# Performance work log

Measured on AMD Instinct MI355X. Metric: run time of the kernel, lower is better.

## Reference

```python
import jax, jax.numpy as jnp
import numpy as np

K = 1_000_000      # number of sparse (2D-det, 3D-anchor) candidate pairs
ROWS = 200         # max 2D detections
COLS = 70400       # number of 3D anchors (200*176*2)
SENTINEL = -9999999.0


def setup_inputs() -> dict:
    key = jax.random.key(0)
    ks = jax.random.split(key, 12)
    input_1 = jax.random.normal(ks[0], (1, 4, 1, K), dtype=jnp.float32)
    idx0 = jax.random.randint(ks[1], (K,), 0, ROWS)
    idx1 = jax.random.randint(ks[2], (K,), 0, COLS)
    tensor_index = jnp.stack([idx0, idx1], axis=1).astype(jnp.int64)
    # fuse_2d_3d: 1x1 Conv2d stack 4->18->36->36->1 (weights as (out,in) matrices)
    def w(k, o, i):
        return jax.random.normal(k, (o, i), dtype=jnp.float32) * (1.0 / np.sqrt(i))
    return {
        "input_1": input_1,
        "tensor_index": tensor_index,
        "W1": w(ks[3], 18, 4),  "b1": jnp.zeros((18,), jnp.float32),
        "W2": w(ks[4], 36, 18), "b2": jnp.zeros((36,), jnp.float32),
        "W3": w(ks[5], 36, 36), "b3": jnp.zeros((36,), jnp.float32),
        "W4": w(ks[6], 1, 36),  "b4": jnp.zeros((1,), jnp.float32),
    }


def reference(input_1, tensor_index, W1, b1, W2, b2, W3, b3, W4, b4):
    # 1x1 convs over (1,4,1,K) are channel matmuls over the K pair axis.
    x = input_1[0, :, 0, :]                                   # (4, K)
    h = jax.nn.relu(jnp.dot(W1, x) + b1[:, None])             # (18, K)
    h = jax.nn.relu(jnp.dot(W2, h) + b2[:, None])             # (36, K)
    h = jax.nn.relu(jnp.dot(W3, h) + b3[:, None])             # (36, K)
    v = (jnp.dot(W4, h) + b4[:, None])[0]                     # (K,) fused score per pair
    # Scatter into dense sentinel-filled grid, then max-reduce the 200 dim
    # (equivalent to MaxPool2d([200,1]) in the original).
    dense = jnp.full((ROWS, COLS), SENTINEL, dtype=input_1.dtype)
    dense = dense.at[tensor_index[:, 0], tensor_index[:, 1]].max(v)
    out = jnp.max(dense, axis=0).reshape(1, -1, 1)            # (1, 70400, 1)
    flag = 1
    return (out, flag)
```

## Files before the change

kernel.cpp:

```cpp
#include <hip/hip_runtime.h>

#define KN 1000000
#define NCOLS 70400
#define NTILES (KN / 16)
#define NBLK 1024
#define NTHR 256

typedef _Float16 f16x8 __attribute__((ext_vector_type(8)));
typedef float    f32x4 __attribute__((ext_vector_type(4)));

__device__ __forceinline__ unsigned encodeF(float f) {
    unsigned b = __float_as_uint(f);
    return (b & 0x80000000u) ? ~b : (b | 0x80000000u);
}
__device__ __forceinline__ float decodeF(unsigned e) {
    unsigned b = (e & 0x80000000u) ? (e & 0x7fffffffu) : ~e;
    return __uint_as_float(b);
}
#define ENC_SENT 0x34E76980u

#define LGKM0() asm volatile("s_waitcnt lgkmcnt(0)" ::: "memory")


__global__ __launch_bounds__(NTHR)
__attribute__((amdgpu_waves_per_eu(4, 4)))
void mlp_scatter_mfma(const float* __restrict__ x, const int* __restrict__ tidx,
                      const float* __restrict__ W1, const float* __restrict__ b1,
                      const float* __restrict__ W2, const float* __restrict__ b2,
                      const float* __restrict__ W3, const float* __restrict__ b3,
                      const float* __restrict__ W4, const float* __restrict__ b4,
                      unsigned* __restrict__ outU)
{
    __shared__ _Float16 smem[4][1808];
    __shared__ float vt[4][16];

    const int lane = threadIdx.x & 63;
    const int wv   = threadIdx.x >> 6;
    const int quad = lane >> 4;
    const int n    = lane & 15;

    {
        unsigned* sp = (unsigned*)&smem[wv][0];
#pragma unroll
        for (int i = 0; i < 14; ++i) sp[i * 64 + lane] = 0u;
    }

    auto bf = [&](const float* W, int OUT, int IN, int t, int ks) {
        f16x8 r;
#pragma unroll
        for (int j = 0; j < 8; ++j) {
            int k  = ks * 32 + quad * 8 + j;
            int ng = t * 16 + n;
            float w = (ng < OUT && k < IN) ? W[ng * IN + k] : 0.0f;
            r[j] = (_Float16)w;
        }
        return r;
    };
    const f16x8 B1_0 = bf(W1, 18,  4, 0, 0), B1_1 = bf(W1, 18,  4, 1, 0);
    const f16x8 B2_0 = bf(W2, 36, 18, 0, 0), B2_1 = bf(W2, 36, 18, 1, 0), B2_2 = bf(W2, 36, 18, 2, 0);
    const f16x8 B3_00 = bf(W3, 36, 36, 0, 0), B3_01 = bf(W3, 36, 36, 0, 1);
    const f16x8 B3_10 = bf(W3, 36, 36, 1, 0), B3_11 = bf(W3, 36, 36, 1, 1);
    const f16x8 B3_20 = bf(W3, 36, 36, 2, 0), B3_21 = bf(W3, 36, 36, 2, 1);
    const f16x8 B4_0 = bf(W4,  1, 36, 0, 0), B4_1 = bf(W4,  1, 36, 0, 1);

    const float bias1_0 = b1[n];
    const float bias1_1 = (n < 2) ? b1[16 + n] : 0.0f;
    const float bias2_0 = b2[n], bias2_1 = b2[16 + n];
    const float bias2_2 = (n < 4) ? b2[32 + n] : 0.0f;
    const float bias3_0 = b3[n], bias3_1 = b3[16 + n];
    const float bias3_2 = (n < 4) ? b3[32 + n] : 0.0f;
    const float b4s = b4[0];

    _Float16* H1 = &smem[wv][0];
    _Float16* H2 = &smem[wv][640];

    const int gw = (blockIdx.x * blockDim.x + threadIdx.x) >> 6;
    const int nw = (gridDim.x * blockDim.x) >> 6;

    for (int tile = gw; tile < NTILES; tile += nw) {
        const int kb = tile * 16;

        const float xj0 = x[0 * KN + kb + n];
        const float xj1 = x[1 * KN + kb + n];
        const float xj2 = x[2 * KN + kb + n];
        const float xj3 = x[3 * KN + kb + n];
        f16x8 a1;
#pragma unroll
        for (int j = 0; j < 8; ++j) a1[j] = (_Float16)0.0f;
        if (quad == 0) {
            a1[0] = (_Float16)xj0; a1[1] = (_Float16)xj1;
            a1[2] = (_Float16)xj2; a1[3] = (_Float16)xj3;
        }

        const int col = ((const int2*)tidx)[kb + n].y;

        f32x4 c0 = {bias1_0, bias1_0, bias1_0, bias1_0};
        f32x4 c1 = {bias1_1, bias1_1, bias1_1, bias1_1};
        c0 = __builtin_amdgcn_mfma_f32_16x16x32_f16(a1, B1_0, c0, 0, 0, 0);
        c1 = __builtin_amdgcn_mfma_f32_16x16x32_f16(a1, B1_1, c1, 0, 0, 0);
#pragma unroll
        for (int r = 0; r < 4; ++r) {
            H1[(quad * 4 + r) * 40 + n]      = (_Float16)fmaxf(c0[r], 0.0f);
            H1[(quad * 4 + r) * 40 + 16 + n] = (_Float16)fmaxf(c1[r], 0.0f);
        }
        LGKM0();

        const f16x8 a2 = *(const f16x8*)&H1[n * 40 + quad * 8];
        f32x4 d0 = {bias2_0, bias2_0, bias2_0, bias2_0};
        f32x4 d1 = {bias2_1, bias2_1, bias2_1, bias2_1};
        f32x4 d2 = {bias2_2, bias2_2, bias2_2, bias2_2};
        d0 = __builtin_amdgcn_mfma_f32_16x16x32_f16(a2, B2_0, d0, 0, 0, 0);
        d1 = __builtin_amdgcn_mfma_f32_16x16x32_f16(a2, B2_1, d1, 0, 0, 0);
        d2 = __builtin_amdgcn_mfma_f32_16x16x32_f16(a2, B2_2, d2, 0, 0, 0);
#pragma unroll
        for (int r = 0; r < 4; ++r) {
            H2[(quad * 4 + r) * 72 + n]      = (_Float16)fmaxf(d0[r], 0.0f);
            H2[(quad * 4 + r) * 72 + 16 + n] = (_Float16)fmaxf(d1[r], 0.0f);
            H2[(quad * 4 + r) * 72 + 32 + n] = (_Float16)fmaxf(d2[r], 0.0f);
        }
        LGKM0();

        const f16x8 a30 = *(const f16x8*)&H2[n * 72 + quad * 8];
        const f16x8 a31 = *(const f16x8*)&H2[n * 72 + 32 + quad * 8];
        f32x4 e0 = {bias3_0, bias3_0, bias3_0, bias3_0};
        f32x4 e1 = {bias3_1, bias3_1, bias3_1, bias3_1};
        f32x4 e2 = {bias3_2, bias3_2, bias3_2, bias3_2};
        e0 = __builtin_amdgcn_mfma_f32_16x16x32_f16(a30, B3_00, e0, 0, 0, 0);
        e0 = __builtin_amdgcn_mfma_f32_16x16x32_f16(a31, B3_01, e0, 0, 0, 0);
        e1 = __builtin_amdgcn_mfma_f32_16x16x32_f16(a30, B3_10, e1, 0, 0, 0);
        e1 = __builtin_amdgcn_mfma_f32_16x16x32_f16(a31, B3_11, e1, 0, 0, 0);
        e2 = __builtin_amdgcn_mfma_f32_16x16x32_f16(a30, B3_20, e2, 0, 0, 0);
        e2 = __builtin_amdgcn_mfma_f32_16x16x32_f16(a31, B3_21, e2, 0, 0, 0);
        LGKM0();
#pragma unroll
        for (int r = 0; r < 4; ++r) {
            H2[(quad * 4 + r) * 72 + n]      = (_Float16)fmaxf(e0[r], 0.0f);
            H2[(quad * 4 + r) * 72 + 16 + n] = (_Float16)fmaxf(e1[r], 0.0f);
            H2[(quad * 4 + r) * 72 + 32 + n] = (_Float16)fmaxf(e2[r], 0.0f);
        }
        LGKM0();

        const f16x8 a40 = *(const f16x8*)&H2[n * 72 + quad * 8];
        const f16x8 a41 = *(const f16x8*)&H2[n * 72 + 32 + quad * 8];
        f32x4 f0 = {0.0f, 0.0f, 0.0f, 0.0f};
        f0 = __builtin_amdgcn_mfma_f32_16x16x32_f16(a40, B4_0, f0, 0, 0, 0);
        f0 = __builtin_amdgcn_mfma_f32_16x16x32_f16(a41, B4_1, f0, 0, 0, 0);

        if (n == 0) {
#pragma unroll
            for (int r = 0; r < 4; ++r) vt[wv][quad * 4 + r] = f0[r] + b4s;
        }
        LGKM0();
        const float v = vt[wv][n];
        const unsigned enc = encodeF(v) - ENC_SENT;
        if (lane < 16) atomicMax(&outU[col], enc);
    }
}

__global__ __launch_bounds__(256) void init_kernel(unsigned* __restrict__ outU) {
    int gid = blockIdx.x * blockDim.x + threadIdx.x;
    if (gid < NCOLS) outU[gid] = 0u;
}

__global__ __launch_bounds__(256) void decode_kernel(unsigned* __restrict__ outU,
                                                     int out_size) {
    int gid = blockIdx.x * blockDim.x + threadIdx.x;
    if (gid < out_size) {
        float r = (gid < NCOLS) ? decodeF(outU[gid] + ENC_SENT) : 1.0f;
        ((float*)outU)[gid] = r;
    }
}

extern "C" void kernel_launch(void* const* d_in, const int* in_sizes, int n_in,
                              void* d_out, int out_size, void* d_ws, size_t ws_size,
                              hipStream_t stream) {
    const float* x    = (const float*)d_in[0];
    const int*   tidx = (const int*)d_in[1];
    const float* W1 = (const float*)d_in[2];
    const float* b1 = (const float*)d_in[3];
    const float* W2 = (const float*)d_in[4];
    const float* b2 = (const float*)d_in[5];
    const float* W3 = (const float*)d_in[6];
    const float* b3 = (const float*)d_in[7];
    const float* W4 = (const float*)d_in[8];
    const float* b4 = (const float*)d_in[9];
    unsigned* outU = (unsigned*)d_out;

    init_kernel<<<(NCOLS + 255) / 256, 256, 0, stream>>>(outU);

    mlp_scatter_mfma<<<NBLK, NTHR, 0, stream>>>(
        x, tidx, W1, b1, W2, b2, W3, b3, W4, b4, outU);

    decode_kernel<<<(out_size + 255) / 256, 256, 0, stream>>>(outU, out_size);
}
```

Before: 141.0 us.

## Process two tiles per wave iteration with prefetch and shuffle-based final layer

Each wave now handles a pair of 16-row tiles per loop iteration, interleaving their MFMA chains to raise instruction-level parallelism. It also register-prefetches the next pair's inputs and column indices so global load latency overlaps the current compute. The 36->1 output layer moves off MFMA to per-lane FMAs plus a 16-lane xor-shuffle reduction, which drops the LDS round-trip for final scores and the explicit lgkmcnt waits. The cost is higher register pressure from the doubled accumulators and prefetch registers, under a fixed waves-per-EU setting.

```diff
diff --git a/kernel.cpp b/kernel.cpp
--- a/kernel.cpp
+++ b/kernel.cpp
@@ -2,7 +2,7 @@
 
 #define KN 1000000
 #define NCOLS 70400
-#define NTILES (KN / 16)
+#define NPAIRS (KN / 32)
 #define NBLK 1024
 #define NTHR 256
 
@@ -19,7 +19,7 @@
 }
 #define ENC_SENT 0x34E76980u
 
-#define LGKM0() asm volatile("s_waitcnt lgkmcnt(0)" ::: "memory")
+#define MFMA16(a, b, c) __builtin_amdgcn_mfma_f32_16x16x32_f16((a), (b), (c), 0, 0, 0)
 
 
 __global__ __launch_bounds__(NTHR)
@@ -31,18 +31,20 @@
                       const float* __restrict__ W4, const float* __restrict__ b4,
                       unsigned* __restrict__ outU)
 {
-    __shared__ _Float16 smem[4][1808];
-    __shared__ float vt[4][16];
+    __shared__ _Float16 smem[4][2][1152];
 
     const int lane = threadIdx.x & 63;
     const int wv   = threadIdx.x >> 6;
     const int quad = lane >> 4;
     const int n    = lane & 15;
 
-    {
-        unsigned* sp = (unsigned*)&smem[wv][0];
-#pragma unroll
-        for (int i = 0; i < 14; ++i) sp[i * 64 + lane] = 0u;
+    _Float16* Ha = &smem[wv][0][0];
+    _Float16* Hb = &smem[wv][1][0];
+
+    for (int i = lane; i < 128; i += 64) {
+        const int row = i >> 3, dc = i & 7;
+        ((unsigned*)(Ha + row * 72 + 48))[dc] = 0u;
+        ((unsigned*)(Hb + row * 72 + 48))[dc] = 0u;
     }
 
     auto bf = [&](const float* W, int OUT, int IN, int t, int ks) {
@@ -61,7 +63,6 @@
     const f16x8 B3_00 = bf(W3, 36, 36, 0, 0), B3_01 = bf(W3, 36, 36, 0, 1);
     const f16x8 B3_10 = bf(W3, 36, 36, 1, 0), B3_11 = bf(W3, 36, 36, 1, 1);
     const f16x8 B3_20 = bf(W3, 36, 36, 2, 0), B3_21 = bf(W3, 36, 36, 2, 1);
-    const f16x8 B4_0 = bf(W4,  1, 36, 0, 0), B4_1 = bf(W4,  1, 36, 0, 1);
 
     const float bias1_0 = b1[n];
     const float bias1_1 = (n < 2) ? b1[16 + n] : 0.0f;
@@ -70,90 +71,118 @@
     const float bias3_0 = b3[n], bias3_1 = b3[16 + n];
     const float bias3_2 = (n < 4) ? b3[32 + n] : 0.0f;
     const float b4s = b4[0];
-
-    _Float16* H1 = &smem[wv][0];
-    _Float16* H2 = &smem[wv][640];
+    const float w4_0 = W4[n], w4_1 = W4[16 + n];
+    const float w4_2 = (n < 4) ? W4[32 + n] : 0.0f;
 
     const int gw = (blockIdx.x * blockDim.x + threadIdx.x) >> 6;
     const int nw = (gridDim.x * blockDim.x) >> 6;
 
-    for (int tile = gw; tile < NTILES; tile += nw) {
-        const int kb = tile * 16;
-
-        const float xj0 = x[0 * KN + kb + n];
-        const float xj1 = x[1 * KN + kb + n];
-        const float xj2 = x[2 * KN + kb + n];
-        const float xj3 = x[3 * KN + kb + n];
-        f16x8 a1;
-#pragma unroll
-        for (int j = 0; j < 8; ++j) a1[j] = (_Float16)0.0f;
+    float cxa0, cxa1, cxa2, cxa3, cxb0, cxb1, cxb2, cxb3;
+    int cca = 0, ccb = 0;
+    if (gw < NPAIRS) {
+        const int kb = gw * 32;
+        cxa0 = x[0 * KN + kb + n];      cxb0 = x[0 * KN + kb + 16 + n];
+        cxa1 = x[1 * KN + kb + n];      cxb1 = x[1 * KN + kb + 16 + n];
+        cxa2 = x[2 * KN + kb + n];      cxb2 = x[2 * KN + kb + 16 + n];
+        cxa3 = x[3 * KN + kb + n];      cxb3 = x[3 * KN + kb + 16 + n];
+        cca  = tidx[2 * (kb + n) + 1];  ccb  = tidx[2 * (kb + 16 + n) + 1];
+    }
+
+    for (int p = gw; p < NPAIRS; ) {
+        const int pn = p + nw;
+        const float xa0 = cxa0, xa1 = cxa1, xa2 = cxa2, xa3 = cxa3;
+        const float xb0 = cxb0, xb1 = cxb1, xb2 = cxb2, xb3 = cxb3;
+        const int cola = cca, colb = ccb;
+        if (pn < NPAIRS) {
+            const int kb = pn * 32;
+            cxa0 = x[0 * KN + kb + n];      cxb0 = x[0 * KN + kb + 16 + n];
+            cxa1 = x[1 * KN + kb + n];      cxb1 = x[1 * KN + kb + 16 + n];
+            cxa2 = x[2 * KN + kb + n];      cxb2 = x[2 * KN + kb + 16 + n];
+            cxa3 = x[3 * KN + kb + n];      cxb3 = x[3 * KN + kb + 16 + n];
+            cca  = tidx[2 * (kb + n) + 1];  ccb  = tidx[2 * (kb + 16 + n) + 1];
+        }
+
+        f16x8 a1a = {}, a1b = {};
         if (quad == 0) {
-            a1[0] = (_Float16)xj0; a1[1] = (_Float16)xj1;
-            a1[2] = (_Float16)xj2; a1[3] = (_Float16)xj3;
-        }
-
-        const int col = ((const int2*)tidx)[kb + n].y;
-
-        f32x4 c0 = {bias1_0, bias1_0, bias1_0, bias1_0};
-        f32x4 c1 = {bias1_1, bias1_1, bias1_1, bias1_1};
-        c0 = __builtin_amdgcn_mfma_f32_16x16x32_f16(a1, B1_0, c0, 0, 0, 0);
-        c1 = __builtin_amdgcn_mfma_f32_16x16x32_f16(a1, B1_1, c1, 0, 0, 0);
+            a1a[0] = (_Float16)xa0; a1a[1] = (_Float16)xa1;
+            a1a[2] = (_Float16)xa2; a1a[3] = (_Float16)xa3;
+            a1b[0] = (_Float16)xb0; a1b[1] = (_Float16)xb1;
+            a1b[2] = (_Float16)xb2; a1b[3] = (_Float16)xb3;
+        }
+        f32x4 c0a = {bias1_0, bias1_0, bias1_0, bias1_0};
+        f32x4 c1a = {bias1_1, bias1_1, bias1_1, bias1_1};
+        f32x4 c0b = c0a, c1b = c1a;
+        c0a = MFMA16(a1a, B1_0, c0a);  c0b = MFMA16(a1b, B1_0, c0b);
+        c1a = MFMA16(a1a, B1_1, c1a);  c1b = MFMA16(a1b, B1_1, c1b);
 #pragma unroll
         for (int r = 0; r < 4; ++r) {
-            H1[(quad * 4 + r) * 40 + n]      = (_Float16)fmaxf(c0[r], 0.0f);
-            H1[(quad * 4 + r) * 40 + 16 + n] = (_Float16)fmaxf(c1[r], 0.0f);
-        }
-        LGKM0();
-
-        const f16x8 a2 = *(const f16x8*)&H1[n * 40 + quad * 8];
-        f32x4 d0 = {bias2_0, bias2_0, bias2_0, bias2_0};
-        f32x4 d1 = {bias2_1, bias2_1, bias2_1, bias2_1};
-        f32x4 d2 = {bias2_2, bias2_2, bias2_2, bias2_2};
-        d0 = __builtin_amdgcn_mfma_f32_16x16x32_f16(a2, B2_0, d0, 0, 0, 0);
-        d1 = __builtin_amdgcn_mfma_f32_16x16x32_f16(a2, B2_1, d1, 0, 0, 0);
-        d2 = __builtin_amdgcn_mfma_f32_16x16x32_f16(a2, B2_2, d2, 0, 0, 0);
+            const int row = (quad * 4 + r) * 72;
+            Ha[row + n]      = (_Float16)fmaxf(c0a[r], 0.0f);
+            Ha[row + 16 + n] = (_Float16)fmaxf(c1a[r], 0.0f);
+            Hb[row + n]      = (_Float16)fmaxf(c0b[r], 0.0f);
+            Hb[row + 16 + n] = (_Float16)fmaxf(c1b[r], 0.0f);
+        }
+
+        const f16x8 a2a = *(const f16x8*)&Ha[n * 72 + quad * 8];
+        const f16x8 a2b = *(const f16x8*)&Hb[n * 72 + quad * 8];
+        f32x4 d0a = {bias2_0, bias2_0, bias2_0, bias2_0};
+        f32x4 d1a = {bias2_1, bias2_1, bias2_1, bias2_1};
+        f32x4 d2a = {bias2_2, bias2_2, bias2_2, bias2_2};
+        f32x4 d0b = d0a, d1b = d1a, d2b = d2a;
+        d0a = MFMA16(a2a, B2_0, d0a);  d0b = MFMA16(a2b, B2_0, d0b);
+        d1a = MFMA16(a2a, B2_1, d1a);  d1b = MFMA16(a2b, B2_1, d1b);
+        d2a = MFMA16(a2a, B2_2, d2a);  d2b = MFMA16(a2b, B2_2, d2b);
 #pragma unroll
         for (int r = 0; r < 4; ++r) {
-            H2[(quad * 4 + r) * 72 + n]      = (_Float16)fmaxf(d0[r], 0.0f);
-            H2[(quad * 4 + r) * 72 + 16 + n] = (_Float16)fmaxf(d1[r], 0.0f);
-            H2[(quad * 4 + r) * 72 + 32 + n] = (_Float16)fmaxf(d2[r], 0.0f);
-        }
-        LGKM0();
-
-        const f16x8 a30 = *(const f16x8*)&H2[n * 72 + quad * 8];
-        const f16x8 a31 = *(const f16x8*)&H2[n * 72 + 32 + quad * 8];
-        f32x4 e0 = {bias3_0, bias3_0, bias3_0, bias3_0};
-        f32x4 e1 = {bias3_1, bias3_1, bias3_1, bias3_1};
-        f32x4 e2 = {bias3_2, bias3_2, bias3_2, bias3_2};
-        e0 = __builtin_amdgcn_mfma_f32_16x16x32_f16(a30, B3_00, e0, 0, 0, 0);
-        e0 = __builtin_amdgcn_mfma_f32_16x16x32_f16(a31, B3_01, e0, 0, 0, 0);
-        e1 = __builtin_amdgcn_mfma_f32_16x16x32_f16(a30, B3_10, e1, 0, 0, 0);
-        e1 = __builtin_amdgcn_mfma_f32_16x16x32_f16(a31, B3_11, e1, 0, 0, 0);
-        e2 = __builtin_amdgcn_mfma_f32_16x16x32_f16(a30, B3_20, e2, 0, 0, 0);
-        e2 = __builtin_amdgcn_mfma_f32_16x16x32_f16(a31, B3_21, e2, 0, 0, 0);
-        LGKM0();
+            const int row = (quad * 4 + r) * 72;
+            Ha[row + n]      = (_Float16)fmaxf(d0a[r], 0.0f);
+            Ha[row + 16 + n] = (_Float16)fmaxf(d1a[r], 0.0f);
+            Ha[row + 32 + n] = (_Float16)fmaxf(d2a[r], 0.0f);
+            Hb[row + n]      = (_Float16)fmaxf(d0b[r], 0.0f);
+            Hb[row + 16 + n] = (_Float16)fmaxf(d1b[r], 0.0f);
+            Hb[row + 32 + n] = (_Float16)fmaxf(d2b[r], 0.0f);
+        }
+
+        const f16x8 a30a = *(const f16x8*)&Ha[n * 72 + quad * 8];
+        const f16x8 a31a = *(const f16x8*)&Ha[n * 72 + 32 + quad * 8];
+        const f16x8 a30b = *(const f16x8*)&Hb[n * 72 + quad * 8];
+        const f16x8 a31b = *(const f16x8*)&Hb[n * 72 + 32 + quad * 8];
+        f32x4 e0a = {bias3_0, bias3_0, bias3_0, bias3_0};
+        f32x4 e1a = {bias3_1, bias3_1, bias3_1, bias3_1};
+        f32x4 e2a = {bias3_2, bias3_2, bias3_2, bias3_2};
+        f32x4 e0b = e0a, e1b = e1a, e2b = e2a;
+        e0a = MFMA16(a30a, B3_00, e0a);  e0a = MFMA16(a31a, B3_01, e0a);
+        e1a = MFMA16(a30a, B3_10, e1a);  e1a = MFMA16(a31a, B3_11, e1a);
+        e2a = MFMA16(a30a, B3_20, e2a);  e2a = MFMA16(a31a, B3_21, e2a);
+        e0b = MFMA16(a30b, B3_00, e0b);  e0b = MFMA16(a31b, B3_01, e0b);
+        e1b = MFMA16(a30b, B3_10, e1b);  e1b = MFMA16(a31b, B3_11, e1b);
+        e2b = MFMA16(a30b, B3_20, e2b);  e2b = MFMA16(a31b, B3_21, e2b);
+
+        float pa[4], pb[4];
 #pragma unroll
         for (int r = 0; r < 4; ++r) {
-            H2[(quad * 4 + r) * 72 + n]      = (_Float16)fmaxf(e0[r], 0.0f);
-            H2[(quad * 4 + r) * 72 + 16 + n] = (_Float16)fmaxf(e1[r], 0.0f);
-            H2[(quad * 4 + r) * 72 + 32 + n] = (_Float16)fmaxf(e2[r], 0.0f);
-        }
-        LGKM0();
-
-        const f16x8 a40 = *(const f16x8*)&H2[n * 72 + quad * 8];
-        const f16x8 a41 = *(const f16x8*)&H2[n * 72 + 32 + quad * 8];
-        f32x4 f0 = {0.0f, 0.0f, 0.0f, 0.0f};
-        f0 = __builtin_amdgcn_mfma_f32_16x16x32_f16(a40, B4_0, f0, 0, 0, 0);
-        f0 = __builtin_amdgcn_mfma_f32_16x16x32_f16(a41, B4_1, f0, 0, 0, 0);
-
-        if (n == 0) {
-#pragma unroll
-            for (int r = 0; r < 4; ++r) vt[wv][quad * 4 + r] = f0[r] + b4s;
-        }
-        LGKM0();
-        const float v = vt[wv][n];
-        const unsigned enc = encodeF(v) - ENC_SENT;
-        if (lane < 16) atomicMax(&outU[col], enc);
+            pa[r] = fmaf(w4_0, fmaxf(e0a[r], 0.0f),
+                    fmaf(w4_1, fmaxf(e1a[r], 0.0f),
+                         w4_2 * fmaxf(e2a[r], 0.0f)));
+            pb[r] = fmaf(w4_0, fmaxf(e0b[r], 0.0f),
+                    fmaf(w4_1, fmaxf(e1b[r], 0.0f),
+                         w4_2 * fmaxf(e2b[r], 0.0f)));
+        }
+#pragma unroll
+        for (int m = 8; m >= 1; m >>= 1) {
+#pragma unroll
+            for (int r = 0; r < 4; ++r) {
+                pa[r] += __shfl_xor(pa[r], m, 16);
+                pb[r] += __shfl_xor(pb[r], m, 16);
+            }
+        }
+        if ((n >> 2) == quad) {
+            const int r = n & 3;
+            atomicMax(&outU[cola], encodeF(pa[r] + b4s) - ENC_SENT);
+            atomicMax(&outU[colb], encodeF(pb[r] + b4s) - ENC_SENT);
+        }
+
+        p = pn;
     }
 }
 
```

Measured after the change: 138.7 us. Within noise of the previous version (-1.7%).
